# Optimization experiments

Hardware: AMD Instinct MI355X
Metric: run time of the kernel (lower is better)

Reference implementation:

```python
import jax, jax.numpy as jnp
import numpy as np

B, S, H = 32, 64, 512
ATT = 128


def _window_index_tables(seq_len):
    # Enumerate all contiguous windows of size 2..S, same set (order-independent
    # for the softmax-weighted sum) as the torch double loop.
    starts, ends = [], []
    for w in range(2, seq_len + 1):
        for s in range(0, seq_len - w + 1):
            starts.append(s)
            ends.append(s + w)
    starts = np.asarray(starts, np.int32)
    ends = np.asarray(ends, np.int32)
    widths = ends - starts
    ks = np.floor(np.log2(widths)).astype(np.int32)  # sparse-table level per window
    e2 = ends - (1 << ks)                            # second gather position
    return starts, e2, ks


def setup_inputs() -> dict:
    key = jax.random.key(0)
    k0, k1, k2, k3, k4 = jax.random.split(key, 5)
    return {
        "lstm_out": jax.random.normal(k0, (B, S, H), dtype=jnp.float32),
        "W1": jax.random.normal(k1, (H, ATT), dtype=jnp.float32) * 0.05,
        "b1": jax.random.normal(k2, (ATT,), dtype=jnp.float32) * 0.05,
        "W2": jax.random.normal(k3, (ATT, 1), dtype=jnp.float32) * 0.05,
        "b2": jax.random.normal(k4, (1,), dtype=jnp.float32) * 0.05,
    }


def reference(lstm_out, W1, b1, W2, b2):
    b, s, h = lstm_out.shape
    # Sparse table: M[k][:, i] = max over lstm_out[:, i : i+2^k] (clipped to s).
    n_levels = int(np.floor(np.log2(s))) + 1
    tables = [lstm_out]
    for k in range(1, n_levels):
        half = 1 << (k - 1)
        prev = tables[-1]
        shifted = jnp.concatenate(
            [prev[:, half:], jnp.full((b, half, h), -jnp.inf, prev.dtype)], axis=1)
        tables.append(jnp.maximum(prev, shifted))
    Mstack = jnp.stack(tables)  # [K, B, S, H]

    starts, e2, ks = _window_index_tables(s)
    # Range max of each window = max of two overlapping power-of-two blocks.
    pooled = jnp.maximum(Mstack[ks, :, starts], Mstack[ks, :, e2])  # [n_win, B, H]
    pooled = jnp.transpose(pooled, (1, 0, 2))  # [B, n_win, H]

    hid = jax.nn.relu(jnp.einsum("bnh,ha->bna", pooled, W1) + b1)
    scores = jnp.einsum("bna,ao->bno", hid, W2) + b2  # [B, n_win, 1]
    attn = jax.nn.softmax(scores, axis=1)
    return jnp.sum(attn * pooled, axis=1)  # [B, H]
```

## Files before the change

### kernel.cpp

```cpp
#include <hip/hip_runtime.h>
#include <stdint.h>


typedef unsigned short u16;
typedef unsigned int u32;

#define B_    32
#define S_    64
#define H_    512
#define ATT_  128
#define NWIN  2016
#define NLEV  7
#define TLEV  6

typedef __bf16 bf16x8 __attribute__((ext_vector_type(8)));
typedef float  f32x4  __attribute__((ext_vector_type(4)));

__device__ __forceinline__ float asf(u32 i) {
  union { u32 i; float f; } v; v.i = i; return v.f;
}
__device__ __forceinline__ u32 asu(float f) {
  union { float f; u32 i; } v; v.f = f; return v.i;
}
__device__ __forceinline__ float bf2f(u16 u) { return asf(((u32)u) << 16); }
__device__ __forceinline__ u16 f2bf(float f) {
  u32 i = asu(f);
  i += 0x7fffu + ((i >> 16) & 1u);
  return (u16)(i >> 16);
}
__device__ __forceinline__ u32 bfmax2(u32 a, u32 b) {
  float a0 = asf(a << 16), a1 = asf(a & 0xffff0000u);
  float b0 = asf(b << 16), b1 = asf(b & 0xffff0000u);
  u32 m0 = asu(fmaxf(a0, b0)), m1 = asu(fmaxf(a1, b1));
  return (m1 & 0xffff0000u) | (m0 >> 16);
}
__device__ __forceinline__ uint4 bfmax8(uint4 a, uint4 b) {
  uint4 m;
  m.x = bfmax2(a.x, b.x); m.y = bfmax2(a.y, b.y);
  m.z = bfmax2(a.z, b.z); m.w = bfmax2(a.w, b.w);
  return m;
}
__device__ __forceinline__ bf16x8 as_bf16x8(uint4 v) {
  union { uint4 u; bf16x8 h; } c; c.u = v; return c.h;
}

__launch_bounds__(256)
__global__ void k01_init(const float* __restrict__ lstm, const float* __restrict__ W1,
                         u16* __restrict__ table, u16* __restrict__ w1t,
                         u16* __restrict__ widx) {
  int bid = blockIdx.x, tid = threadIdx.x;
  __shared__ u16 bufA[64 * 64], bufB[64 * 64];
  if (bid < 256) {
    int hc = bid & 7, b = bid >> 3;
    const float* src = lstm + (size_t)b * S_ * H_ + hc * 64;
    u16* tb = table + (size_t)b * TLEV * S_ * H_ + hc * 64;
    for (int t = tid; t < 64 * 16; t += 256) {
      int r = t >> 4, c4 = t & 15;
      float4 f = *reinterpret_cast<const float4*>(src + r * H_ + c4 * 4);
      ushort4 u;
      u.x = f2bf(f.x); u.y = f2bf(f.y); u.z = f2bf(f.z); u.w = f2bf(f.w);
      *reinterpret_cast<ushort4*>(&bufA[r * 64 + c4 * 4]) = u;
    }
    u16* pa = bufA; u16* pb = bufB;
    for (int k = 1; k < NLEV; ++k) {
      __syncthreads();
      int half = 1 << (k - 1);
      u16* dst_g = tb + (size_t)(k - 1) * S_ * H_;
      for (int t = tid; t < 64 * 16; t += 256) {
        int r = t >> 4, c4 = t & 15;
        int r2 = r + half; if (r2 > 63) r2 = 63;
        uint2 a  = *reinterpret_cast<const uint2*>(&pa[r  * 64 + c4 * 4]);
        uint2 bq = *reinterpret_cast<const uint2*>(&pa[r2 * 64 + c4 * 4]);
        uint2 m; m.x = bfmax2(a.x, bq.x); m.y = bfmax2(a.y, bq.y);
        *reinterpret_cast<uint2*>(&pb[r * 64 + c4 * 4]) = m;
        *reinterpret_cast<uint2*>(dst_g + r * H_ + c4 * 4) = m;
      }
      u16* tmp = pa; pa = pb; pb = tmp;
    }
  } else {
    int gb = bid - 256;
    if (gb == 0) {
      for (int n = tid; n < NWIN; n += 256) {
        int w = 2, rem = n;
        while (rem >= 65 - w) { rem -= 65 - w; ++w; }
        int s = rem;
        int k = 31 - __clz(w);
        int e2 = s + w - (1 << k);
        widx[n] = (u16)(s | (e2 << 6) | (k << 12));
      }
    }
    for (int q = tid; q < 2048; q += 256) {
      int idx = gb * 2048 + q;
      int n = idx >> 9, kq = idx & 511;
      w1t[idx] = f2bf(W1[kq * ATT_ + n]);
    }
  }
}

__launch_bounds__(256, 1)
__global__ void k2_scores(const u16* __restrict__ table, const u16* __restrict__ w1t,
                          const float* __restrict__ b1, const float* __restrict__ w2,
                          const u16* __restrict__ widx, float* __restrict__ scores) {
  const int b = blockIdx.y, mt = blockIdx.x;
  __shared__ u16 Ts[2][128 * 64];
  __shared__ u16 Bs[2][128 * 64];
  __shared__ u16 widx_l[256];
  __shared__ float b1s[128], w2s[128];
  int tid = threadIdx.x;
  {
    int n = mt * 256 + tid; if (n > NWIN - 1) n = NWIN - 1;
    widx_l[tid] = widx[n];
  }
  if (tid < 128) { b1s[tid] = b1[tid]; w2s[tid] = w2[tid]; }
  __syncthreads();

  const int lv_lo = widx_l[0] >> 12;
  const u16* tb = table + (size_t)b * TLEV * S_ * H_ + (size_t)(lv_lo - 1) * S_ * H_;

  const u16* gT[4]; const u16* gB[4]; int sl[4];
#pragma unroll
  for (int p = 0; p < 4; ++p) {
    int slot = p * 256 + tid;
    int r = slot >> 3, c = slot & 7;
    int csw = (c ^ (r & 7)) * 8;
    gT[p] = tb  + r * H_ + csw;
    gB[p] = w1t + r * H_ + csw;
    sl[p] = slot * 8;
  }

#define DMA(KC, BSEL) do {                                                     \
    int ko_ = (KC) * 64;                                                       \
    _Pragma("unroll")                                                          \
    for (int p_ = 0; p_ < 4; ++p_) {                                           \
      __builtin_amdgcn_global_load_lds(                                        \
          (const __attribute__((address_space(1))) void*)(gT[p_] + ko_),       \
          (__attribute__((address_space(3))) void*)(&Ts[(BSEL)][sl[p_]]),      \
          16, 0, 0);                                                           \
      __builtin_amdgcn_global_load_lds(                                        \
          (const __attribute__((address_space(1))) void*)(gB[p_] + ko_),       \
          (__attribute__((address_space(3))) void*)(&Bs[(BSEL)][sl[p_]]),      \
          16, 0, 0);                                                           \
    }                                                                          \
  } while (0)

  int wid = tid >> 6, lane = tid & 63;
  int lrow = lane & 15, quad = lane >> 4;

  int aoff[4][2][2];
#pragma unroll
  for (int mi = 0; mi < 4; ++mi) {
    int pk = widx_l[wid * 64 + mi * 16 + lrow];
    int s = pk & 63, e2 = (pk >> 6) & 63, lv = (pk >> 12) - lv_lo;
    int rs = lv * 64 + s, re = lv * 64 + e2;
#pragma unroll
    for (int k2i = 0; k2i < 2; ++k2i) {
      int c = quad + k2i * 4;
      aoff[mi][k2i][0] = rs * 64 + ((c ^ (rs & 7)) * 8);
      aoff[mi][k2i][1] = re * 64 + ((c ^ (re & 7)) * 8);
    }
  }
  int boff[8][2];
#pragma unroll
  for (int j = 0; j < 8; ++j) {
    int n = j * 16 + lrow;
#pragma unroll
    for (int k2i = 0; k2i < 2; ++k2i) {
      int c = quad + k2i * 4;
      boff[j][k2i] = n * 64 + ((c ^ (n & 7)) * 8);
    }
  }

  f32x4 acc[4][8];
#pragma unroll
  for (int mi = 0; mi < 4; ++mi)
#pragma unroll
    for (int j = 0; j < 8; ++j) acc[mi][j] = (f32x4){0.f, 0.f, 0.f, 0.f};

  DMA(0, 0);

  for (int kc = 0; kc < 8; ++kc) {
    __syncthreads();
    if (kc < 7) DMA(kc + 1, (kc + 1) & 1);
    const u16* Tc = Ts[kc & 1];
    const u16* Bc = Bs[kc & 1];
#pragma unroll
    for (int k2i = 0; k2i < 2; ++k2i) {
      bf16x8 bfr[8];
#pragma unroll
      for (int j = 0; j < 8; ++j)
        bfr[j] = *reinterpret_cast<const bf16x8*>(&Bc[boff[j][k2i]]);
#pragma unroll
      for (int mi = 0; mi < 4; ++mi) {
        uint4 va = *reinterpret_cast<const uint4*>(&Tc[aoff[mi][k2i][0]]);
        uint4 vb = *reinterpret_cast<const uint4*>(&Tc[aoff[mi][k2i][1]]);
        bf16x8 af = as_bf16x8(bfmax8(va, vb));
#pragma unroll
        for (int j = 0; j < 8; ++j)
          acc[mi][j] = __builtin_amdgcn_mfma_f32_16x16x32_bf16(af, bfr[j], acc[mi][j], 0, 0, 0);
      }
    }
  }
#undef DMA

#pragma unroll
  for (int mi = 0; mi < 4; ++mi) {
#pragma unroll
    for (int r = 0; r < 4; ++r) {
      float p = 0.f;
#pragma unroll
      for (int j = 0; j < 8; ++j) {
        int n = j * 16 + lrow;
        float v = acc[mi][j][r] + b1s[n];
        p += (v > 0.f ? v : 0.f) * w2s[n];
      }
      p += __shfl_xor(p, 1, 16);
      p += __shfl_xor(p, 2, 16);
      p += __shfl_xor(p, 4, 16);
      p += __shfl_xor(p, 8, 16);
      if (lrow == 0) {
        int nw = mt * 256 + wid * 64 + mi * 16 + quad * 4 + r;
        if (nw < NWIN) scores[b * NWIN + nw] = p;
      }
    }
  }
}

__launch_bounds__(256)
__global__ void k34_out(const u16* __restrict__ table, const float* __restrict__ scores,
                        const u16* __restrict__ widx, float* __restrict__ out) {
  int hc = blockIdx.x, b = blockIdx.y, tid = threadIdx.x;
  __shared__ u16 Tl[6 * 64 * 32];
  __shared__ float attn_l[NWIN];
  __shared__ u16 widx_l[NWIN];
  __shared__ float red[8][32];
  __shared__ float wredM[4], wredS[4];
  const u16* tb = table + (size_t)b * TLEV * S_ * H_;
  int h0 = hc * 32;
  int lane = tid & 63, wid = tid >> 6;

  for (int t = tid; t < 6 * 64 * 4; t += 256) {
    int row = t >> 2, c = t & 3;
    uint4 v = *reinterpret_cast<const uint4*>(tb + row * H_ + h0 + c * 8);
    *reinterpret_cast<uint4*>(&Tl[row * 32 + c * 8]) = v;
  }
  for (int n = tid; n < NWIN; n += 256) widx_l[n] = widx[n];

  float mx = -1e30f;
  for (int n = tid; n < NWIN; n += 256) {
    float v = scores[b * NWIN + n];
    attn_l[n] = v;
    mx = fmaxf(mx, v);
  }
#pragma unroll
  for (int off = 32; off > 0; off >>= 1) mx = fmaxf(mx, __shfl_xor(mx, off, 64));
  if (lane == 0) wredM[wid] = mx;
  __syncthreads();
  mx = fmaxf(fmaxf(wredM[0], wredM[1]), fmaxf(wredM[2], wredM[3]));
  float sum = 0.f;
  for (int n = tid; n < NWIN; n += 256) {
    float e = __expf(attn_l[n] - mx);
    attn_l[n] = e;
    sum += e;
  }
#pragma unroll
  for (int off = 32; off > 0; off >>= 1) sum += __shfl_xor(sum, off, 64);
  if (lane == 0) wredS[wid] = sum;
  __syncthreads();
  float inv = 1.f / (wredS[0] + wredS[1] + wredS[2] + wredS[3]);

  int h = tid & 31, g = tid >> 5;
  float acc = 0.f;
  for (int n = g * 252; n < g * 252 + 252; ++n) {
    int pk = widx_l[n];
    int s = pk & 63, e2 = (pk >> 6) & 63, lv = pk >> 12;
    float va = bf2f(Tl[((lv - 1) * 64 + s) * 32 + h]);
    float vb = bf2f(Tl[((lv - 1) * 64 + e2) * 32 + h]);
    acc += attn_l[n] * fmaxf(va, vb);
  }
  red[g][h] = acc;
  __syncthreads();
  if (tid < 32) {
    float s2 = 0.f;
#pragma unroll
    for (int g2 = 0; g2 < 8; ++g2) s2 += red[g2][tid];
    out[b * H_ + h0 + tid] = s2 * inv;
  }
}

extern "C" void kernel_launch(void* const* d_in, const int* in_sizes, int n_in,
                              void* d_out, int out_size, void* d_ws, size_t ws_size,
                              hipStream_t stream) {
  const float* lstm = (const float*)d_in[0];
  const float* W1   = (const float*)d_in[1];
  const float* b1   = (const float*)d_in[2];
  const float* W2   = (const float*)d_in[3];
  float* out = (float*)d_out;

  char* ws = (char*)d_ws;
  u16*   widx   = (u16*)(ws + 0);
  u16*   w1t    = (u16*)(ws + 4096);
  u16*   table  = (u16*)(ws + 135168);
  float* scores = (float*)(ws + 12718080);

  k01_init <<<288, 256, 0, stream>>>(lstm, W1, table, w1t, widx);
  k2_scores<<<dim3(8, B_), 256, 0, stream>>>(table, w1t, b1, W2, widx, scores);
  k34_out  <<<dim3(16, B_), 256, 0, stream>>>(table, scores, widx, out);
}
```

Baseline: 118.8 us.

## Widen output kernel to 64 columns with vectorized swizzled LDS reads; fold init work

The output kernel now handles 64 hidden columns per block instead of 32. Each thread reads 8 bf16 values per window as one 16-byte LDS load from an XOR-swizzled table and keeps 8 accumulators, with cross-lane shuffles replacing part of the shared-memory reduction. This cuts the number of per-window index and attention loads and the LDS instruction count, but halves the block count to 256. The init kernel also drops its 32 extra blocks and spreads the W1 transpose and window-index setup across the sparse-table blocks.

```diff
diff --git a/kernel.cpp b/kernel.cpp
--- a/kernel.cpp
+++ b/kernel.cpp
@@ -50,50 +50,49 @@
                          u16* __restrict__ widx) {
   int bid = blockIdx.x, tid = threadIdx.x;
   __shared__ u16 bufA[64 * 64], bufB[64 * 64];
-  if (bid < 256) {
-    int hc = bid & 7, b = bid >> 3;
-    const float* src = lstm + (size_t)b * S_ * H_ + hc * 64;
-    u16* tb = table + (size_t)b * TLEV * S_ * H_ + hc * 64;
+
+  {
+    int idx = bid * 256 + tid;
+    int n = idx >> 9, kq = idx & 511;
+    w1t[idx] = f2bf(W1[kq * ATT_ + n]);
+  }
+  if (bid < 8) {
+    int n = bid * 256 + tid;
+    if (n < NWIN) {
+      int w = 2, rem = n;
+      while (rem >= 65 - w) { rem -= 65 - w; ++w; }
+      int s = rem;
+      int k = 31 - __clz(w);
+      int e2 = s + w - (1 << k);
+      widx[n] = (u16)(s | (e2 << 6) | (k << 12));
+    }
+  }
+
+  int hc = bid & 7, b = bid >> 3;
+  const float* src = lstm + (size_t)b * S_ * H_ + hc * 64;
+  u16* tb = table + (size_t)b * TLEV * S_ * H_ + hc * 64;
+  for (int t = tid; t < 64 * 16; t += 256) {
+    int r = t >> 4, c4 = t & 15;
+    float4 f = *reinterpret_cast<const float4*>(src + r * H_ + c4 * 4);
+    ushort4 u;
+    u.x = f2bf(f.x); u.y = f2bf(f.y); u.z = f2bf(f.z); u.w = f2bf(f.w);
+    *reinterpret_cast<ushort4*>(&bufA[r * 64 + c4 * 4]) = u;
+  }
+  u16* pa = bufA; u16* pb = bufB;
+  for (int k = 1; k < NLEV; ++k) {
+    __syncthreads();
+    int half = 1 << (k - 1);
+    u16* dst_g = tb + (size_t)(k - 1) * S_ * H_;
     for (int t = tid; t < 64 * 16; t += 256) {
       int r = t >> 4, c4 = t & 15;
-      float4 f = *reinterpret_cast<const float4*>(src + r * H_ + c4 * 4);
-      ushort4 u;
-      u.x = f2bf(f.x); u.y = f2bf(f.y); u.z = f2bf(f.z); u.w = f2bf(f.w);
-      *reinterpret_cast<ushort4*>(&bufA[r * 64 + c4 * 4]) = u;
-    }
-    u16* pa = bufA; u16* pb = bufB;
-    for (int k = 1; k < NLEV; ++k) {
-      __syncthreads();
-      int half = 1 << (k - 1);
-      u16* dst_g = tb + (size_t)(k - 1) * S_ * H_;
-      for (int t = tid; t < 64 * 16; t += 256) {
-        int r = t >> 4, c4 = t & 15;
-        int r2 = r + half; if (r2 > 63) r2 = 63;
-        uint2 a  = *reinterpret_cast<const uint2*>(&pa[r  * 64 + c4 * 4]);
-        uint2 bq = *reinterpret_cast<const uint2*>(&pa[r2 * 64 + c4 * 4]);
-        uint2 m; m.x = bfmax2(a.x, bq.x); m.y = bfmax2(a.y, bq.y);
-        *reinterpret_cast<uint2*>(&pb[r * 64 + c4 * 4]) = m;
-        *reinterpret_cast<uint2*>(dst_g + r * H_ + c4 * 4) = m;
-      }
-      u16* tmp = pa; pa = pb; pb = tmp;
-    }
-  } else {
-    int gb = bid - 256;
-    if (gb == 0) {
-      for (int n = tid; n < NWIN; n += 256) {
-        int w = 2, rem = n;
-        while (rem >= 65 - w) { rem -= 65 - w; ++w; }
-        int s = rem;
-        int k = 31 - __clz(w);
-        int e2 = s + w - (1 << k);
-        widx[n] = (u16)(s | (e2 << 6) | (k << 12));
-      }
-    }
-    for (int q = tid; q < 2048; q += 256) {
-      int idx = gb * 2048 + q;
-      int n = idx >> 9, kq = idx & 511;
-      w1t[idx] = f2bf(W1[kq * ATT_ + n]);
-    }
+      int r2 = r + half; if (r2 > 63) r2 = 63;
+      uint2 a  = *reinterpret_cast<const uint2*>(&pa[r  * 64 + c4 * 4]);
+      uint2 bq = *reinterpret_cast<const uint2*>(&pa[r2 * 64 + c4 * 4]);
+      uint2 m; m.x = bfmax2(a.x, bq.x); m.y = bfmax2(a.y, bq.y);
+      *reinterpret_cast<uint2*>(&pb[r * 64 + c4 * 4]) = m;
+      *reinterpret_cast<uint2*>(dst_g + r * H_ + c4 * 4) = m;
+    }
+    u16* tmp = pa; pa = pb; pb = tmp;
   }
 }
 
@@ -229,19 +228,19 @@
 __global__ void k34_out(const u16* __restrict__ table, const float* __restrict__ scores,
                         const u16* __restrict__ widx, float* __restrict__ out) {
   int hc = blockIdx.x, b = blockIdx.y, tid = threadIdx.x;
-  __shared__ u16 Tl[6 * 64 * 32];
+  __shared__ u16 Tl[TLEV * 64 * 64];
   __shared__ float attn_l[NWIN];
   __shared__ u16 widx_l[NWIN];
-  __shared__ float red[8][32];
+  __shared__ float red[4][64];
   __shared__ float wredM[4], wredS[4];
   const u16* tb = table + (size_t)b * TLEV * S_ * H_;
-  int h0 = hc * 32;
+  int h0 = hc * 64;
   int lane = tid & 63, wid = tid >> 6;
 
-  for (int t = tid; t < 6 * 64 * 4; t += 256) {
-    int row = t >> 2, c = t & 3;
+  for (int t = tid; t < TLEV * 64 * 8; t += 256) {
+    int row = t >> 3, c = t & 7;
     uint4 v = *reinterpret_cast<const uint4*>(tb + row * H_ + h0 + c * 8);
-    *reinterpret_cast<uint4*>(&Tl[row * 32 + c * 8]) = v;
+    *reinterpret_cast<uint4*>(&Tl[row * 64 + ((c ^ (row & 7)) * 8)]) = v;
   }
   for (int n = tid; n < NWIN; n += 256) widx_l[n] = widx[n];
 
@@ -268,21 +267,45 @@
   __syncthreads();
   float inv = 1.f / (wredS[0] + wredS[1] + wredS[2] + wredS[3]);
 
-  int h = tid & 31, g = tid >> 5;
-  float acc = 0.f;
-  for (int n = g * 252; n < g * 252 + 252; ++n) {
+  int hq = tid & 7, g = tid >> 3;
+  float acc[8];
+#pragma unroll
+  for (int j = 0; j < 8; ++j) acc[j] = 0.f;
+  for (int i = 0; i < 63; ++i) {
+    int n = g * 63 + i;
     int pk = widx_l[n];
+    float a = attn_l[n];
     int s = pk & 63, e2 = (pk >> 6) & 63, lv = pk >> 12;
-    float va = bf2f(Tl[((lv - 1) * 64 + s) * 32 + h]);
-    float vb = bf2f(Tl[((lv - 1) * 64 + e2) * 32 + h]);
-    acc += attn_l[n] * fmaxf(va, vb);
-  }
-  red[g][h] = acc;
+    int rs = (lv - 1) * 64 + s, re = (lv - 1) * 64 + e2;
+    uint4 va = *reinterpret_cast<const uint4*>(&Tl[rs * 64 + ((hq ^ (rs & 7)) * 8)]);
+    uint4 vb = *reinterpret_cast<const uint4*>(&Tl[re * 64 + ((hq ^ (re & 7)) * 8)]);
+    u32 ua, ub;
+#define ACC2(UA, UB, J0) do {                                            \
+      float xa0 = asf((UA) << 16), xa1 = asf((UA) & 0xffff0000u);        \
+      float xb0 = asf((UB) << 16), xb1 = asf((UB) & 0xffff0000u);        \
+      acc[(J0)]     = fmaf(a, fmaxf(xa0, xb0), acc[(J0)]);               \
+      acc[(J0) + 1] = fmaf(a, fmaxf(xa1, xb1), acc[(J0) + 1]);           \
+    } while (0)
+    ua = va.x; ub = vb.x; ACC2(ua, ub, 0);
+    ua = va.y; ub = vb.y; ACC2(ua, ub, 2);
+    ua = va.z; ub = vb.z; ACC2(ua, ub, 4);
+    ua = va.w; ub = vb.w; ACC2(ua, ub, 6);
+#undef ACC2
+  }
+
+#pragma unroll
+  for (int j = 0; j < 8; ++j) {
+    acc[j] += __shfl_xor(acc[j], 8, 64);
+    acc[j] += __shfl_xor(acc[j], 16, 64);
+    acc[j] += __shfl_xor(acc[j], 32, 64);
+  }
+  if (lane < 8) {
+#pragma unroll
+    for (int j = 0; j < 8; ++j) red[wid][hq * 8 + j] = acc[j];
+  }
   __syncthreads();
-  if (tid < 32) {
-    float s2 = 0.f;
-#pragma unroll
-    for (int g2 = 0; g2 < 8; ++g2) s2 += red[g2][tid];
+  if (tid < 64) {
+    float s2 = red[0][tid] + red[1][tid] + red[2][tid] + red[3][tid];
     out[b * H_ + h0 + tid] = s2 * inv;
   }
 }
@@ -302,7 +325,7 @@
   u16*   table  = (u16*)(ws + 135168);
   float* scores = (float*)(ws + 12718080);
 
-  k01_init <<<288, 256, 0, stream>>>(lstm, W1, table, w1t, widx);
+  k01_init <<<256, 256, 0, stream>>>(lstm, W1, table, w1t, widx);
   k2_scores<<<dim3(8, B_), 256, 0, stream>>>(table, w1t, b1, W2, widx, scores);
-  k34_out  <<<dim3(16, B_), 256, 0, stream>>>(table, scores, widx, out);
-}
+  k34_out  <<<dim3(8, B_), 256, 0, stream>>>(table, scores, widx, out);
+}
```

After: 116.0 us, median of 2. -2.3%, faster.
